# Kernel optimization log

Hardware: AMD Instinct MI355X
Metric: run time of the kernel (lower is better)

Reference implementation:

```python
import jax, jax.numpy as jnp
import numpy as np

B, S, D, H = 4, 2048, 1024, 16
DK = D // H


def setup_inputs() -> dict:
    key = jax.random.key(0)
    ks = jax.random.split(key, 12)
    std = 0.02
    inp = {
        "q": jax.random.normal(ks[0], (B, S, D), jnp.float32),
        "k": jax.random.normal(ks[1], (B, S, D), jnp.float32),
        "v": jax.random.normal(ks[2], (B, S, D), jnp.float32),
        # causal mask: 1 above diagonal (positions to be masked with -inf)
        "mask": jnp.triu(jnp.ones((S, S), jnp.int32), k=1)[None, None, :, :],
        "Wq": jax.random.normal(ks[3], (D, D), jnp.float32) * std,
        "bq": jnp.zeros((D,), jnp.float32),
        "Wk": jax.random.normal(ks[4], (D, D), jnp.float32) * std,
        "bk": jnp.zeros((D,), jnp.float32),
        "Wv": jax.random.normal(ks[5], (D, D), jnp.float32) * std,
        "bv": jnp.zeros((D,), jnp.float32),
        "Wo": jax.random.normal(ks[6], (D, D), jnp.float32) * std,
        "bo": jnp.zeros((D,), jnp.float32),
    }
    return inp


def _split_heads(x):
    b, s, d = x.shape
    return x.reshape(b, s, H, DK).transpose(0, 2, 1, 3)  # [B,H,S,DK]


def reference(q, k, v, mask, Wq, bq, Wk, bk, Wv, bv, Wo, bo):
    # linear projections (torch Linear: x @ W.T + b)
    qh = _split_heads(q @ Wq.T + bq)
    kh = _split_heads(k @ Wk.T + bk)
    vh = _split_heads(v @ Wv.T + bv)
    scale = 1.0 / jnp.sqrt(jnp.asarray(DK, qh.dtype))
    scores = jnp.einsum("bhqd,bhkd->bhqk", qh, kh) * scale
    scores = jnp.where(mask == 1, -jnp.inf, scores)
    attn = jax.nn.softmax(scores, axis=-1)
    # dropout is identity in eval mode (deterministic reference)
    out = jnp.einsum("bhqk,bhkd->bhqd", attn, vh)
    concat = out.transpose(0, 2, 1, 3).reshape(q.shape[0], -1, D)
    return concat @ Wo.T + bo
```

## Files before the change

kernel.cpp:

```cpp
#include <hip/hip_runtime.h>
#include <hip/hip_bf16.h>

#define BB  4
#define SS  2048
#define DD  1024
#define HH  16
#define DKK 64

typedef unsigned short u16;
typedef short v8s __attribute__((ext_vector_type(8)));
typedef short v4s __attribute__((ext_vector_type(4)));
typedef float v4f __attribute__((ext_vector_type(4)));
typedef float v16f __attribute__((ext_vector_type(16)));
typedef unsigned int v4u __attribute__((ext_vector_type(4)));

#define MFMA32(a, b, c) __builtin_amdgcn_mfma_f32_32x32x16_bf16(a, b, c, 0, 0, 0)

__device__ __forceinline__ u16 f2b(float x) {
  unsigned int u = __float_as_uint(x);
  unsigned int r = (u + 0x7fffu + ((u >> 16) & 1u)) >> 16;
  return (u16)r;
}

__device__ __forceinline__ unsigned int pkhalf(float a, float b) {
  return __builtin_amdgcn_perm(__float_as_uint(a), __float_as_uint(b), 0x03020706u);
}

__device__ __forceinline__ void gload16(const u16* g, u16* l) {
  __builtin_amdgcn_global_load_lds(
      (const __attribute__((address_space(1))) void*)g,
      (__attribute__((address_space(3))) void*)l, 16, 0, 0);
}

__device__ __forceinline__ void cvt8(const float* in, u16* out, size_t j) {
  const float4* p = (const float4*)(in + j * 8);
  float4 a = p[0], b = p[1];
  v8s r = {(short)f2b(a.x), (short)f2b(a.y), (short)f2b(a.z), (short)f2b(a.w),
           (short)f2b(b.x), (short)f2b(b.y), (short)f2b(b.z), (short)f2b(b.w)};
  *(v8s*)(out + j * 8) = r;
}

__global__ void cvt3(const float* __restrict__ q, const float* __restrict__ k,
                     const float* __restrict__ v, u16* __restrict__ x0,
                     u16* __restrict__ x1, u16* __restrict__ x2) {
  int i = blockIdx.x * blockDim.x + threadIdx.x;
  int which = i >> 20;
  size_t j = (size_t)(i & 0xFFFFF);
  const float* s = which == 0 ? q : (which == 1 ? k : v);
  u16* d = which == 0 ? x0 : (which == 1 ? x1 : x2);
  cvt8(s, d, j);
}

__global__ void cvtW(const float* __restrict__ a, const float* __restrict__ b,
                     const float* __restrict__ c, const float* __restrict__ d,
                     u16* __restrict__ oa, u16* __restrict__ ob,
                     u16* __restrict__ oc, u16* __restrict__ od) {
  int i = blockIdx.x * blockDim.x + threadIdx.x;
  int which = i >> 17;
  size_t j = (size_t)(i & 0x1FFFF);
  const float* s = which == 0 ? a : (which == 1 ? b : (which == 2 ? c : d));
  u16* o = which == 0 ? oa : (which == 1 ? ob : (which == 2 ? oc : od));
  cvt8(s, o, j);
}

__device__ __forceinline__ void gemm_core(
    const u16* __restrict__ A, const u16* __restrict__ Bw,
    int row0, int col0, u16* As, u16* Bs, v4f acc[4][4]) {
  const int tid = threadIdx.x;
  const int lane = tid & 63, wid = tid >> 6;
  const int wm = wid >> 1, wn = wid & 1;
  const int lr = lane & 15, lg = lane >> 4;

  v4f zero = {0.f, 0.f, 0.f, 0.f};
#pragma unroll
  for (int m = 0; m < 4; ++m)
#pragma unroll
    for (int n = 0; n < 4; ++n) acc[m][n] = zero;

  const int rowoff = wid * 8 + (lane >> 3);
  const int scol = ((lane & 7) ^ ((lane >> 3) & 7)) * 8;
  const u16* gA = A + (size_t)(row0 + rowoff) * DD + scol;
  const u16* gB = Bw + (size_t)(col0 + rowoff) * DD + scol;
  u16* lAb = As + wid * 512;
  u16* lBb = Bs + wid * 512;

#pragma unroll
  for (int i2 = 0; i2 < 4; ++i2) {
    gload16(gA + (size_t)(i2 * 32) * DD, lAb + i2 * 2048);
    gload16(gB + (size_t)(i2 * 32) * DD, lBb + i2 * 2048);
  }
  asm volatile("s_waitcnt vmcnt(0)" ::: "memory");
  __builtin_amdgcn_s_barrier();

  const int a_r0 = (wm * 64 + lr) * 64;
  const int b_r0 = (wn * 64 + lr) * 64;
  const int sl = lr & 7;

  for (int t = 0; t < 16; ++t) {
    const int buf = t & 1;
    if (t < 15) {
      const u16* nA = gA + (size_t)(t + 1) * 64;
      const u16* nB = gB + (size_t)(t + 1) * 64;
      u16* dA = lAb + (buf ^ 1) * 8192;
      u16* dB = lBb + (buf ^ 1) * 8192;
#pragma unroll
      for (int i2 = 0; i2 < 4; ++i2) {
        gload16(nA + (size_t)(i2 * 32) * DD, dA + i2 * 2048);
        gload16(nB + (size_t)(i2 * 32) * DD, dB + i2 * 2048);
      }
    }
    const u16* Ab = As + buf * 8192;
    const u16* Bb = Bs + buf * 8192;
#pragma unroll
    for (int ks = 0; ks < 2; ++ks) {
      v8s af[4], bf[4];
#pragma unroll
      for (int m = 0; m < 4; ++m)
        af[m] = *(const v8s*)(Ab + a_r0 + m * 1024 + (((ks * 4 + lg) ^ sl) * 8));
#pragma unroll
      for (int n = 0; n < 4; ++n)
        bf[n] = *(const v8s*)(Bb + b_r0 + n * 1024 + (((ks * 4 + lg) ^ sl) * 8));
#pragma unroll
      for (int m = 0; m < 4; ++m)
#pragma unroll
        for (int n = 0; n < 4; ++n)
          acc[m][n] = __builtin_amdgcn_mfma_f32_16x16x32_bf16(af[m], bf[n], acc[m][n], 0, 0, 0);
    }
    asm volatile("s_waitcnt vmcnt(0)" ::: "memory");
    __builtin_amdgcn_s_barrier();
  }
}

__global__ __launch_bounds__(256) void gemm_qkv(
    const u16* __restrict__ X0, const u16* __restrict__ X1, const u16* __restrict__ X2,
    const u16* __restrict__ Wqb, const u16* __restrict__ Wkb, const u16* __restrict__ Wvb,
    const float* __restrict__ bq, const float* __restrict__ bk, const float* __restrict__ bv,
    u16* __restrict__ Qp, u16* __restrict__ Kp, u16* __restrict__ VT, float qsc) {
  __shared__ u16 As[2][128][64];
  __shared__ u16 Bs[2][128][64];
  const int z = blockIdx.z;
  const u16* A = z == 0 ? X0 : (z == 1 ? X1 : X2);
  const u16* Bw = z == 0 ? Wqb : (z == 1 ? Wkb : Wvb);
  const float* bias = z == 0 ? bq : (z == 1 ? bk : bv);
  const float oscale = z == 0 ? qsc : 1.0f;
  const int row0 = blockIdx.x * 128, col0 = blockIdx.y * 128;

  v4f acc[4][4];
  gemm_core(A, Bw, row0, col0, &As[0][0][0], &Bs[0][0][0], acc);

  const int tid = threadIdx.x;
  const int lane = tid & 63, wid = tid >> 6;
  const int wm = wid >> 1, wn = wid & 1;
  const int lr = lane & 15, lg = lane >> 4;

  if (z < 2) {
    u16* C = z == 0 ? Qp : Kp;
#pragma unroll
    for (int n = 0; n < 4; ++n) {
      int gc = col0 + wn * 64 + n * 16 + lr;
      float bv2 = bias[gc];
#pragma unroll
      for (int m = 0; m < 4; ++m) {
        int gr0 = row0 + wm * 64 + m * 16 + lg * 4;
#pragma unroll
        for (int r = 0; r < 4; ++r)
          C[(size_t)(gr0 + r) * DD + gc] = f2b((acc[m][n][r] + bv2) * oscale);
      }
    }
  } else {
#pragma unroll
    for (int n = 0; n < 4; ++n) {
      int gc = col0 + wn * 64 + n * 16 + lr;
      float bv2 = bias[gc];
      int h = gc >> 6, dk = gc & 63;
#pragma unroll
      for (int m = 0; m < 4; ++m) {
        int gr0 = row0 + wm * 64 + m * 16 + lg * 4;
        int b = gr0 >> 11;
        int s = gr0 & 2047;
        u16* vbase = VT + (((size_t)b * HH + h) * DKK + dk) * SS + s;
#pragma unroll
        for (int r = 0; r < 4; ++r) vbase[r] = f2b(acc[m][n][r] + bv2);
      }
    }
  }
}

__global__ __launch_bounds__(256) void gemm_out(
    const u16* __restrict__ A, const u16* __restrict__ Bw,
    const float* __restrict__ bias, float* __restrict__ Cp) {
  __shared__ u16 As[2][128][64];
  __shared__ u16 Bs[2][128][64];
  const int row0 = blockIdx.x * 128, col0 = blockIdx.y * 128;

  v4f acc[4][4];
  gemm_core(A, Bw, row0, col0, &As[0][0][0], &Bs[0][0][0], acc);

  const int tid = threadIdx.x;
  const int lane = tid & 63, wid = tid >> 6;
  const int wm = wid >> 1, wn = wid & 1;
  const int lr = lane & 15, lg = lane >> 4;

#pragma unroll
  for (int n = 0; n < 4; ++n) {
    int gc = col0 + wn * 64 + n * 16 + lr;
    float bv2 = bias[gc];
#pragma unroll
    for (int m = 0; m < 4; ++m) {
      int gr0 = row0 + wm * 64 + m * 16 + lg * 4;
#pragma unroll
      for (int r = 0; r < 4; ++r)
        Cp[(size_t)(gr0 + r) * DD + gc] = acc[m][n][r] + bv2;
    }
  }
}

__device__ __forceinline__ void build_pa(const v16f& p, int hi, v8s& a0, v8s& a1) {
  unsigned int u0 = pkhalf(p[0], p[1]);
  unsigned int u1 = pkhalf(p[2], p[3]);
  unsigned int u2 = pkhalf(p[4], p[5]);
  unsigned int u3 = pkhalf(p[6], p[7]);
  unsigned int u4 = pkhalf(p[8], p[9]);
  unsigned int u5 = pkhalf(p[10], p[11]);
  unsigned int u6 = pkhalf(p[12], p[13]);
  unsigned int u7 = pkhalf(p[14], p[15]);
  unsigned int s0 = hi ? u0 : u2;
  unsigned int s1 = hi ? u1 : u3;
  unsigned int s2 = hi ? u4 : u6;
  unsigned int s3 = hi ? u5 : u7;
  unsigned int r0 = __shfl_xor(s0, 32);
  unsigned int r1 = __shfl_xor(s1, 32);
  unsigned int r2 = __shfl_xor(s2, 32);
  unsigned int r3 = __shfl_xor(s3, 32);
  v4u f0 = {hi ? r0 : u0, hi ? r1 : u1, hi ? u2 : r0, hi ? u3 : r1};
  v4u f1 = {hi ? r2 : u4, hi ? r3 : u5, hi ? u6 : r2, hi ? u7 : r3};
  a0 = __builtin_bit_cast(v8s, f0);
  a1 = __builtin_bit_cast(v8s, f1);
}

__global__ __launch_bounds__(256) void attn_fwd5(
    const u16* __restrict__ Qp, const u16* __restrict__ Kp,
    const u16* __restrict__ VT, u16* __restrict__ O) {
  __shared__ u16 Ks[128][72];
  __shared__ u16 Vs[64][136];
  const int tid = threadIdx.x;
  const int w = tid >> 6, lane = tid & 63;
  const int ql = lane & 31;
  const int hi = lane >> 5;
  const int i = blockIdx.x;
  const int dw = i >> 8, sl2 = i & 255;
  const int bh = sl2 & 63, g = sl2 >> 6;
  const int qt = (int)((0x3210674598BACDEFull >> (4 * (dw * 4 + g))) & 15);
  const int b = bh >> 4, h = bh & 15;
  const int q0 = qt * 128;
  const int qw0 = q0 + w * 32;
  const int qg = qw0 + ql;

  v8s qf[4];
  const u16* qbase = Qp + (size_t)(b * SS + qg) * DD + h * DKK + hi * 8;
#pragma unroll
  for (int ks = 0; ks < 4; ++ks) qf[ks] = *(const v8s*)(qbase + ks * 16);

  const int krow = tid >> 3, kcol = (tid & 7) * 8;
  const int vrow = tid >> 4, vcol = (tid & 15) * 8;
  const u16* gK = Kp + (size_t)(b * SS + krow) * DD + h * DKK + kcol;
  const u16* gV = VT + ((size_t)bh * DKK + vrow) * SS + vcol;

  const int nt = qt + 1;
  v8s stK[4], stV[4];
#pragma unroll
  for (int j = 0; j < 4; ++j) stK[j] = *(const v8s*)(gK + (size_t)(32 * j) * DD);
#pragma unroll
  for (int j = 0; j < 4; ++j) stV[j] = *(const v8s*)(gV + (size_t)(16 * j) * SS);

  float l = 0.f;
  v16f o0 = {0, 0, 0, 0, 0, 0, 0, 0, 0, 0, 0, 0, 0, 0, 0, 0};
  v16f o1 = o0;

  for (int t = 0; t < nt; ++t) {
    __syncthreads();
#pragma unroll
    for (int j = 0; j < 4; ++j) *(v8s*)&Ks[krow + 32 * j][kcol] = stK[j];
#pragma unroll
    for (int j = 0; j < 4; ++j) *(v8s*)&Vs[vrow + 16 * j][vcol] = stV[j];
    if (t + 1 < nt) {
      const u16* nK = gK + (size_t)(t + 1) * 128 * DD;
      const u16* nV = gV + (t + 1) * 128;
#pragma unroll
      for (int j = 0; j < 4; ++j) stK[j] = *(const v8s*)(nK + (size_t)(32 * j) * DD);
#pragma unroll
      for (int j = 0; j < 4; ++j) stV[j] = *(const v8s*)(nV + (size_t)(16 * j) * SS);
    }
    __syncthreads();
    const int kv0 = t * 128;

#pragma unroll
    for (int sub = 0; sub < 4; ++sub) {
      const int kvs = kv0 + sub * 32;
      if (kvs > qw0 + 31) break;

      v16f p = {0, 0, 0, 0, 0, 0, 0, 0, 0, 0, 0, 0, 0, 0, 0, 0};
#pragma unroll
      for (int ks = 0; ks < 4; ++ks) {
        v8s a = *(const v8s*)&Ks[sub * 32 + ql][ks * 16 + hi * 8];
        p = MFMA32(a, qf[ks], p);
      }

      if (kvs + 31 > qw0) {
#pragma unroll
        for (int r = 0; r < 16; ++r) {
          int row = (r & 3) + 8 * (r >> 2) + 4 * hi;
          if (kvs + row > qg) p[r] = -3.0e38f;
        }
      }

      float rs = 0.f;
#pragma unroll
      for (int r = 0; r < 16; ++r) {
        p[r] = exp2f(p[r]);
        rs += p[r];
      }
      l += rs;

      v8s pa0, pa1;
      build_pa(p, hi, pa0, pa1);

      __builtin_amdgcn_s_setprio(1);
      o0 = MFMA32(pa0, *(const v8s*)&Vs[ql][sub * 32 + hi * 8], o0);
      o0 = MFMA32(pa1, *(const v8s*)&Vs[ql][sub * 32 + 16 + hi * 8], o0);
      o1 = MFMA32(pa0, *(const v8s*)&Vs[32 + ql][sub * 32 + hi * 8], o1);
      o1 = MFMA32(pa1, *(const v8s*)&Vs[32 + ql][sub * 32 + 16 + hi * 8], o1);
      __builtin_amdgcn_s_setprio(0);
    }
  }

  float lt = l + __shfl_xor(l, 32);
  float linv = 1.f / lt;
#pragma unroll
  for (int r = 0; r < 16; ++r) {
    int row = (r & 3) + 8 * (r >> 2) + 4 * hi;
    float lr2 = __shfl(linv, row);
    size_t obase = (size_t)(b * SS + qw0 + row) * DD + h * DKK + ql;
    O[obase] = f2b(o0[r] * lr2);
    O[obase + 32] = f2b(o1[r] * lr2);
  }
}

extern "C" void kernel_launch(void* const* d_in, const int* in_sizes, int n_in,
                              void* d_out, int out_size, void* d_ws, size_t ws_size,
                              hipStream_t stream) {
  (void)in_sizes; (void)n_in; (void)out_size; (void)ws_size;
  const float* q  = (const float*)d_in[0];
  const float* k  = (const float*)d_in[1];
  const float* v  = (const float*)d_in[2];
  const float* Wq = (const float*)d_in[4];
  const float* bq = (const float*)d_in[5];
  const float* Wk = (const float*)d_in[6];
  const float* bk = (const float*)d_in[7];
  const float* Wv = (const float*)d_in[8];
  const float* bv = (const float*)d_in[9];
  const float* Wo = (const float*)d_in[10];
  const float* bo = (const float*)d_in[11];

  u16* base = (u16*)d_ws;
  const size_t WE = (size_t)DD * DD;
  const size_t PE = (size_t)BB * SS * DD;
  u16* Wq_b = base;
  u16* Wk_b = Wq_b + WE;
  u16* Wv_b = Wk_b + WE;
  u16* Wo_b = Wv_b + WE;
  u16* Qp = Wo_b + WE;
  u16* Kp = Qp + PE;
  u16* X2 = Kp + PE;
  u16* VT = X2 + PE;
  u16* Op = X2;

  u16* X0 = (u16*)d_out;
  u16* X1 = X0 + PE;

  const float qsc = 0.125f * 1.44269504f;

  cvtW<<<2048, 256, 0, stream>>>(Wq, Wk, Wv, Wo, Wq_b, Wk_b, Wv_b, Wo_b);
  cvt3<<<12288, 256, 0, stream>>>(q, k, v, X0, X1, X2);

  dim3 gq(64, 8, 3);
  gemm_qkv<<<gq, 256, 0, stream>>>(X0, X1, X2, Wq_b, Wk_b, Wv_b,
                                   bq, bk, bv, Qp, Kp, VT, qsc);

  attn_fwd5<<<1024, 256, 0, stream>>>(Qp, Kp, VT, Op);

  dim3 go(64, 8);
  gemm_out<<<go, 256, 0, stream>>>(Op, Wo_b, bo, (float*)d_out);
}
```

Measured before the change: 210.2 us.

## Replace QKV projection GEMM with 256x256-tile, 8-wave pipelined kernel

Swaps the 128x128-tile QKV projection GEMM for a new kernel using 256x256 tiles, 512 threads and a 128KB shared buffer. Global loads for the next K-step are issued in quarter-steps interleaved with the MFMA phases, with fine-grained waitcnt/barriers and raised wave priority around the MFMAs. This is meant to improve operand reuse and overlap loads with compute. The trade-off is a grid of only 384 blocks with one block per CU, which risks tail imbalance and lower occupancy.

Measured after the change: 210.1 us. No clear change (-0.0%).

```diff
diff --git a/kernel.cpp b/kernel.cpp
--- a/kernel.cpp
+++ b/kernel.cpp
@@ -63,6 +63,130 @@
   cvt8(s, o, j);
 }
 
+__global__ __launch_bounds__(512) void gemm_qkv256(
+    const u16* __restrict__ X0, const u16* __restrict__ X1, const u16* __restrict__ X2,
+    const u16* __restrict__ Wqb, const u16* __restrict__ Wkb, const u16* __restrict__ Wvb,
+    const float* __restrict__ bq, const float* __restrict__ bk, const float* __restrict__ bv,
+    u16* __restrict__ Qp, u16* __restrict__ Kp, u16* __restrict__ VT, float qsc) {
+  __shared__ u16 S[65536];
+  const int z = blockIdx.z;
+  const u16* A = z == 0 ? X0 : (z == 1 ? X1 : X2);
+  const u16* Bw = z == 0 ? Wqb : (z == 1 ? Wkb : Wvb);
+  const float* bias = z == 0 ? bq : (z == 1 ? bk : bv);
+  const float oscale = z == 0 ? qsc : 1.0f;
+  const int row0 = blockIdx.x * 256, col0 = blockIdx.y * 256;
+
+  const int tid = threadIdx.x;
+  const int lane = tid & 63, wid = tid >> 6;
+  const int wm = wid >> 2, wn = wid & 3;
+  const int lr = lane & 15, lg = lane >> 4;
+
+  v4f acc[8][4];
+  v4f zero = {0.f, 0.f, 0.f, 0.f};
+#pragma unroll
+  for (int i = 0; i < 8; ++i)
+#pragma unroll
+    for (int j = 0; j < 4; ++j) acc[i][j] = zero;
+
+  const int srow = tid >> 2;
+  const int schunk = (tid & 3) * 8;
+  auto stage = [&](const u16* G, int grow0, int kc, int halfbase) {
+#pragma unroll
+    for (int r2 = 0; r2 < 2; ++r2) {
+      gload16(G + (size_t)(grow0 + r2 * 128 + srow) * DD + kc + schunk,
+              S + halfbase + (r2 * 512 + wid * 64) * 8);
+    }
+  };
+
+  stage(A, row0, 0, 0);
+  stage(Bw, col0, 0, 32768);
+  stage(A, row0, 32, 8192);
+  stage(Bw, col0, 32, 32768 + 8192);
+  asm volatile("s_waitcnt vmcnt(4)" ::: "memory");
+  __builtin_amdgcn_s_barrier();
+
+  for (int t = 0; t < 16; ++t) {
+    const int buf = t & 1;
+    const int ab = buf * 16384;
+    const int bb = 32768 + buf * 16384;
+    const int nab = (buf ^ 1) * 16384;
+    const int nbb = 32768 + (buf ^ 1) * 16384;
+    const int kn = (t + 1) * 64;
+    v8s bf[4];
+#pragma unroll
+    for (int p = 0; p < 4; ++p) {
+      const int ks = p >> 1, mh = p & 1;
+      v8s af[4];
+      {
+        const u16* Ab = S + ab + ks * 8192 + (wm * 128 + mh * 64 + lr) * 32 + lg * 8;
+#pragma unroll
+        for (int i = 0; i < 4; ++i) af[i] = *(const v8s*)(Ab + i * 512);
+      }
+      if (mh == 0) {
+        const u16* Bb = S + bb + ks * 8192 + (wn * 64 + lr) * 32 + lg * 8;
+#pragma unroll
+        for (int nf = 0; nf < 4; ++nf) bf[nf] = *(const v8s*)(Bb + nf * 512);
+      }
+      if (t < 15) {
+        if (p == 0)      stage(A,  row0, kn,      nab);
+        else if (p == 1) stage(Bw, col0, kn,      nbb);
+        else if (p == 2) stage(A,  row0, kn + 32, nab + 8192);
+        else             stage(Bw, col0, kn + 32, nbb + 8192);
+      }
+      __builtin_amdgcn_s_barrier();
+      asm volatile("s_waitcnt lgkmcnt(0)" ::: "memory");
+      __builtin_amdgcn_sched_barrier(0);
+      __builtin_amdgcn_s_setprio(1);
+#pragma unroll
+      for (int i = 0; i < 4; ++i)
+#pragma unroll
+        for (int nf = 0; nf < 4; ++nf)
+          acc[mh * 4 + i][nf] = __builtin_amdgcn_mfma_f32_16x16x32_bf16(
+              af[i], bf[nf], acc[mh * 4 + i][nf], 0, 0, 0);
+      __builtin_amdgcn_s_setprio(0);
+      if (p == 1) {
+        if (t < 15) asm volatile("s_waitcnt vmcnt(4)" ::: "memory");
+        else        asm volatile("s_waitcnt vmcnt(0)" ::: "memory");
+      } else if (p == 3) {
+        if (t < 15) asm volatile("s_waitcnt vmcnt(4)" ::: "memory");
+      }
+      __builtin_amdgcn_s_barrier();
+    }
+  }
+
+  if (z < 2) {
+    u16* C = z == 0 ? Qp : Kp;
+#pragma unroll
+    for (int nf = 0; nf < 4; ++nf) {
+      int gc = col0 + wn * 64 + nf * 16 + lr;
+      float bv2 = bias[gc];
+#pragma unroll
+      for (int mf = 0; mf < 8; ++mf) {
+        int gr0 = row0 + wm * 128 + mf * 16 + lg * 4;
+#pragma unroll
+        for (int r = 0; r < 4; ++r)
+          C[(size_t)(gr0 + r) * DD + gc] = f2b((acc[mf][nf][r] + bv2) * oscale);
+      }
+    }
+  } else {
+#pragma unroll
+    for (int nf = 0; nf < 4; ++nf) {
+      int gc = col0 + wn * 64 + nf * 16 + lr;
+      float bv2 = bias[gc];
+      int h = gc >> 6, dk = gc & 63;
+#pragma unroll
+      for (int mf = 0; mf < 8; ++mf) {
+        int gr0 = row0 + wm * 128 + mf * 16 + lg * 4;
+        int b = gr0 >> 11;
+        int s = gr0 & 2047;
+        u16* vbase = VT + (((size_t)b * HH + h) * DKK + dk) * SS + s;
+#pragma unroll
+        for (int r = 0; r < 4; ++r) vbase[r] = f2b(acc[mf][nf][r] + bv2);
+      }
+    }
+  }
+}
+
 __device__ __forceinline__ void gemm_core(
     const u16* __restrict__ A, const u16* __restrict__ Bw,
     int row0, int col0, u16* As, u16* Bs, v4f acc[4][4]) {
@@ -128,61 +252,6 @@
     }
     asm volatile("s_waitcnt vmcnt(0)" ::: "memory");
     __builtin_amdgcn_s_barrier();
-  }
-}
-
-__global__ __launch_bounds__(256) void gemm_qkv(
-    const u16* __restrict__ X0, const u16* __restrict__ X1, const u16* __restrict__ X2,
-    const u16* __restrict__ Wqb, const u16* __restrict__ Wkb, const u16* __restrict__ Wvb,
-    const float* __restrict__ bq, const float* __restrict__ bk, const float* __restrict__ bv,
-    u16* __restrict__ Qp, u16* __restrict__ Kp, u16* __restrict__ VT, float qsc) {
-  __shared__ u16 As[2][128][64];
-  __shared__ u16 Bs[2][128][64];
-  const int z = blockIdx.z;
-  const u16* A = z == 0 ? X0 : (z == 1 ? X1 : X2);
-  const u16* Bw = z == 0 ? Wqb : (z == 1 ? Wkb : Wvb);
-  const float* bias = z == 0 ? bq : (z == 1 ? bk : bv);
-  const float oscale = z == 0 ? qsc : 1.0f;
-  const int row0 = blockIdx.x * 128, col0 = blockIdx.y * 128;
-
-  v4f acc[4][4];
-  gemm_core(A, Bw, row0, col0, &As[0][0][0], &Bs[0][0][0], acc);
-
-  const int tid = threadIdx.x;
-  const int lane = tid & 63, wid = tid >> 6;
-  const int wm = wid >> 1, wn = wid & 1;
-  const int lr = lane & 15, lg = lane >> 4;
-
-  if (z < 2) {
-    u16* C = z == 0 ? Qp : Kp;
-#pragma unroll
-    for (int n = 0; n < 4; ++n) {
-      int gc = col0 + wn * 64 + n * 16 + lr;
-      float bv2 = bias[gc];
-#pragma unroll
-      for (int m = 0; m < 4; ++m) {
-        int gr0 = row0 + wm * 64 + m * 16 + lg * 4;
-#pragma unroll
-        for (int r = 0; r < 4; ++r)
-          C[(size_t)(gr0 + r) * DD + gc] = f2b((acc[m][n][r] + bv2) * oscale);
-      }
-    }
-  } else {
-#pragma unroll
-    for (int n = 0; n < 4; ++n) {
-      int gc = col0 + wn * 64 + n * 16 + lr;
-      float bv2 = bias[gc];
-      int h = gc >> 6, dk = gc & 63;
-#pragma unroll
-      for (int m = 0; m < 4; ++m) {
-        int gr0 = row0 + wm * 64 + m * 16 + lg * 4;
-        int b = gr0 >> 11;
-        int s = gr0 & 2047;
-        u16* vbase = VT + (((size_t)b * HH + h) * DKK + dk) * SS + s;
-#pragma unroll
-        for (int r = 0; r < 4; ++r) vbase[r] = f2b(acc[m][n][r] + bv2);
-      }
-    }
   }
 }
 
@@ -383,9 +452,9 @@
   cvtW<<<2048, 256, 0, stream>>>(Wq, Wk, Wv, Wo, Wq_b, Wk_b, Wv_b, Wo_b);
   cvt3<<<12288, 256, 0, stream>>>(q, k, v, X0, X1, X2);
 
-  dim3 gq(64, 8, 3);
-  gemm_qkv<<<gq, 256, 0, stream>>>(X0, X1, X2, Wq_b, Wk_b, Wv_b,
-                                   bq, bk, bv, Qp, Kp, VT, qsc);
+  dim3 gq(32, 4, 3);
+  gemm_qkv256<<<gq, 512, 0, stream>>>(X0, X1, X2, Wq_b, Wk_b, Wv_b,
+                                      bq, bk, bv, Qp, Kp, VT, qsc);
 
   attn_fwd5<<<1024, 256, 0, stream>>>(Qp, Kp, VT, Op);
 
```

## Fuse fp32-to-bf16 activation conversion into QKV projection GEMM

Applied to the files above, without the earlier changes.

Removes the separate cvt3 kernel that converted q, k and v to bf16 in a workspace. The new gemm_qkvf kernel loads fp32 activations directly, converts them in registers and stores bf16 tiles to LDS, with a K-tile of 32 and a register-prefetch double buffer. This drops a full write and re-read of the bf16 activations and one launch. In exchange the A tile is now staged through registers instead of async global-to-LDS loads, the K step is smaller so there are more barriers per block, and each fp32 A tile is reread by all 8 column blocks.

Result: slower. 221.8 us (+5.5%).

```diff
diff --git a/kernel.cpp b/kernel.cpp
--- a/kernel.cpp
+++ b/kernel.cpp
@@ -38,17 +38,6 @@
   v8s r = {(short)f2b(a.x), (short)f2b(a.y), (short)f2b(a.z), (short)f2b(a.w),
            (short)f2b(b.x), (short)f2b(b.y), (short)f2b(b.z), (short)f2b(b.w)};
   *(v8s*)(out + j * 8) = r;
-}
-
-__global__ void cvt3(const float* __restrict__ q, const float* __restrict__ k,
-                     const float* __restrict__ v, u16* __restrict__ x0,
-                     u16* __restrict__ x1, u16* __restrict__ x2) {
-  int i = blockIdx.x * blockDim.x + threadIdx.x;
-  int which = i >> 20;
-  size_t j = (size_t)(i & 0xFFFFF);
-  const float* s = which == 0 ? q : (which == 1 ? k : v);
-  u16* d = which == 0 ? x0 : (which == 1 ? x1 : x2);
-  cvt8(s, d, j);
 }
 
 __global__ void cvtW(const float* __restrict__ a, const float* __restrict__ b,
@@ -63,6 +52,122 @@
   cvt8(s, o, j);
 }
 
+__global__ __launch_bounds__(256) void gemm_qkvf(
+    const float* __restrict__ Xq, const float* __restrict__ Xk, const float* __restrict__ Xv,
+    const u16* __restrict__ Wqb, const u16* __restrict__ Wkb, const u16* __restrict__ Wvb,
+    const float* __restrict__ bq, const float* __restrict__ bk, const float* __restrict__ bv,
+    u16* __restrict__ Qp, u16* __restrict__ Kp, u16* __restrict__ VT, float qsc) {
+  __shared__ u16 As[2][128][32];
+  __shared__ u16 Bs[2][128][32];
+  const int z = blockIdx.z;
+  const float* A = z == 0 ? Xq : (z == 1 ? Xk : Xv);
+  const u16* Bw = z == 0 ? Wqb : (z == 1 ? Wkb : Wvb);
+  const float* bias = z == 0 ? bq : (z == 1 ? bk : bv);
+  const float oscale = z == 0 ? qsc : 1.0f;
+  const int row0 = blockIdx.x * 128, col0 = blockIdx.y * 128;
+
+  const int tid = threadIdx.x;
+  const int lane = tid & 63, wid = tid >> 6;
+  const int wm = wid >> 1, wn = wid & 1;
+  const int lr = lane & 15, lg = lane >> 4;
+
+  v4f zero = {0.f, 0.f, 0.f, 0.f};
+  v4f acc[4][4];
+#pragma unroll
+  for (int m = 0; m < 4; ++m)
+#pragma unroll
+    for (int n = 0; n < 4; ++n) acc[m][n] = zero;
+
+  const int ar = tid >> 1, ah = tid & 1;
+  const float4* gA = (const float4*)(A + (size_t)(row0 + ar) * DD) + ah * 4;
+  const int e0 = wid * 128 + lane;
+  const int e1 = e0 + 64;
+  const u16* gB0 = Bw + (size_t)(col0 + (e0 >> 2)) * DD + (e0 & 3) * 8;
+  const u16* gB1 = Bw + (size_t)(col0 + (e1 >> 2)) * DD + (e1 & 3) * 8;
+  u16* lB0 = &Bs[0][0][0] + (2 * wid + 0) * 512;
+  u16* lB1 = &Bs[0][0][0] + (2 * wid + 1) * 512;
+
+  {
+    float4 pa0 = gA[0], pa1 = gA[1], pa2 = gA[2], pa3 = gA[3];
+    gload16(gB0, lB0);
+    gload16(gB1, lB1);
+    v8s w0 = {(short)f2b(pa0.x), (short)f2b(pa0.y), (short)f2b(pa0.z), (short)f2b(pa0.w),
+              (short)f2b(pa1.x), (short)f2b(pa1.y), (short)f2b(pa1.z), (short)f2b(pa1.w)};
+    v8s w1 = {(short)f2b(pa2.x), (short)f2b(pa2.y), (short)f2b(pa2.z), (short)f2b(pa2.w),
+              (short)f2b(pa3.x), (short)f2b(pa3.y), (short)f2b(pa3.z), (short)f2b(pa3.w)};
+    *(v8s*)&As[0][ar][ah * 16] = w0;
+    *(v8s*)&As[0][ar][ah * 16 + 8] = w1;
+  }
+  asm volatile("s_waitcnt vmcnt(0) lgkmcnt(0)" ::: "memory");
+  __builtin_amdgcn_s_barrier();
+
+  for (int t = 0; t < 32; ++t) {
+    const int buf = t & 1;
+    float4 na0{}, na1{}, na2{}, na3{};
+    if (t < 31) {
+      const float4* g = gA + (t + 1) * 8;
+      na0 = g[0]; na1 = g[1]; na2 = g[2]; na3 = g[3];
+      gload16(gB0 + (t + 1) * 32, lB0 + (buf ^ 1) * 4096);
+      gload16(gB1 + (t + 1) * 32, lB1 + (buf ^ 1) * 4096);
+    }
+
+    v8s af[4], bf[4];
+#pragma unroll
+    for (int m = 0; m < 4; ++m) af[m] = *(const v8s*)&As[buf][wm * 64 + m * 16 + lr][lg * 8];
+#pragma unroll
+    for (int n = 0; n < 4; ++n) bf[n] = *(const v8s*)&Bs[buf][wn * 64 + n * 16 + lr][lg * 8];
+#pragma unroll
+    for (int m = 0; m < 4; ++m)
+#pragma unroll
+      for (int n = 0; n < 4; ++n)
+        acc[m][n] = __builtin_amdgcn_mfma_f32_16x16x32_bf16(af[m], bf[n], acc[m][n], 0, 0, 0);
+
+    if (t < 31) {
+      v8s w0 = {(short)f2b(na0.x), (short)f2b(na0.y), (short)f2b(na0.z), (short)f2b(na0.w),
+                (short)f2b(na1.x), (short)f2b(na1.y), (short)f2b(na1.z), (short)f2b(na1.w)};
+      v8s w1 = {(short)f2b(na2.x), (short)f2b(na2.y), (short)f2b(na2.z), (short)f2b(na2.w),
+                (short)f2b(na3.x), (short)f2b(na3.y), (short)f2b(na3.z), (short)f2b(na3.w)};
+      *(v8s*)&As[buf ^ 1][ar][ah * 16] = w0;
+      *(v8s*)&As[buf ^ 1][ar][ah * 16 + 8] = w1;
+      asm volatile("s_waitcnt vmcnt(0)" ::: "memory");
+    }
+    asm volatile("s_waitcnt lgkmcnt(0)" ::: "memory");
+    __builtin_amdgcn_s_barrier();
+  }
+
+  if (z < 2) {
+    u16* C = z == 0 ? Qp : Kp;
+#pragma unroll
+    for (int n = 0; n < 4; ++n) {
+      int gc = col0 + wn * 64 + n * 16 + lr;
+      float bv2 = bias[gc];
+#pragma unroll
+      for (int m = 0; m < 4; ++m) {
+        int gr0 = row0 + wm * 64 + m * 16 + lg * 4;
+#pragma unroll
+        for (int r = 0; r < 4; ++r)
+          C[(size_t)(gr0 + r) * DD + gc] = f2b((acc[m][n][r] + bv2) * oscale);
+      }
+    }
+  } else {
+#pragma unroll
+    for (int n = 0; n < 4; ++n) {
+      int gc = col0 + wn * 64 + n * 16 + lr;
+      float bv2 = bias[gc];
+      int h = gc >> 6, dk = gc & 63;
+#pragma unroll
+      for (int m = 0; m < 4; ++m) {
+        int gr0 = row0 + wm * 64 + m * 16 + lg * 4;
+        int b = gr0 >> 11;
+        int s = gr0 & 2047;
+        u16* vbase = VT + (((size_t)b * HH + h) * DKK + dk) * SS + s;
+#pragma unroll
+        for (int r = 0; r < 4; ++r) vbase[r] = f2b(acc[m][n][r] + bv2);
+      }
+    }
+  }
+}
+
 __device__ __forceinline__ void gemm_core(
     const u16* __restrict__ A, const u16* __restrict__ Bw,
     int row0, int col0, u16* As, u16* Bs, v4f acc[4][4]) {
@@ -128,61 +233,6 @@
     }
     asm volatile("s_waitcnt vmcnt(0)" ::: "memory");
     __builtin_amdgcn_s_barrier();
-  }
-}
-
-__global__ __launch_bounds__(256) void gemm_qkv(
-    const u16* __restrict__ X0, const u16* __restrict__ X1, const u16* __restrict__ X2,
-    const u16* __restrict__ Wqb, const u16* __restrict__ Wkb, const u16* __restrict__ Wvb,
-    const float* __restrict__ bq, const float* __restrict__ bk, const float* __restrict__ bv,
-    u16* __restrict__ Qp, u16* __restrict__ Kp, u16* __restrict__ VT, float qsc) {
-  __shared__ u16 As[2][128][64];
-  __shared__ u16 Bs[2][128][64];
-  const int z = blockIdx.z;
-  const u16* A = z == 0 ? X0 : (z == 1 ? X1 : X2);
-  const u16* Bw = z == 0 ? Wqb : (z == 1 ? Wkb : Wvb);
-  const float* bias = z == 0 ? bq : (z == 1 ? bk : bv);
-  const float oscale = z == 0 ? qsc : 1.0f;
-  const int row0 = blockIdx.x * 128, col0 = blockIdx.y * 128;
-
-  v4f acc[4][4];
-  gemm_core(A, Bw, row0, col0, &As[0][0][0], &Bs[0][0][0], acc);
-
-  const int tid = threadIdx.x;
-  const int lane = tid & 63, wid = tid >> 6;
-  const int wm = wid >> 1, wn = wid & 1;
-  const int lr = lane & 15, lg = lane >> 4;
-
-  if (z < 2) {
-    u16* C = z == 0 ? Qp : Kp;
-#pragma unroll
-    for (int n = 0; n < 4; ++n) {
-      int gc = col0 + wn * 64 + n * 16 + lr;
-      float bv2 = bias[gc];
-#pragma unroll
-      for (int m = 0; m < 4; ++m) {
-        int gr0 = row0 + wm * 64 + m * 16 + lg * 4;
-#pragma unroll
-        for (int r = 0; r < 4; ++r)
-          C[(size_t)(gr0 + r) * DD + gc] = f2b((acc[m][n][r] + bv2) * oscale);
-      }
-    }
-  } else {
-#pragma unroll
-    for (int n = 0; n < 4; ++n) {
-      int gc = col0 + wn * 64 + n * 16 + lr;
-      float bv2 = bias[gc];
-      int h = gc >> 6, dk = gc & 63;
-#pragma unroll
-      for (int m = 0; m < 4; ++m) {
-        int gr0 = row0 + wm * 64 + m * 16 + lg * 4;
-        int b = gr0 >> 11;
-        int s = gr0 & 2047;
-        u16* vbase = VT + (((size_t)b * HH + h) * DKK + dk) * SS + s;
-#pragma unroll
-        for (int r = 0; r < 4; ++r) vbase[r] = f2b(acc[m][n][r] + bv2);
-      }
-    }
   }
 }
 
@@ -371,21 +421,16 @@
   u16* Wo_b = Wv_b + WE;
   u16* Qp = Wo_b + WE;
   u16* Kp = Qp + PE;
-  u16* X2 = Kp + PE;
-  u16* VT = X2 + PE;
-  u16* Op = X2;
-
-  u16* X0 = (u16*)d_out;
-  u16* X1 = X0 + PE;
+  u16* Op = Kp + PE;
+  u16* VT = Op + PE;
 
   const float qsc = 0.125f * 1.44269504f;
 
   cvtW<<<2048, 256, 0, stream>>>(Wq, Wk, Wv, Wo, Wq_b, Wk_b, Wv_b, Wo_b);
-  cvt3<<<12288, 256, 0, stream>>>(q, k, v, X0, X1, X2);
 
   dim3 gq(64, 8, 3);
-  gemm_qkv<<<gq, 256, 0, stream>>>(X0, X1, X2, Wq_b, Wk_b, Wv_b,
-                                   bq, bk, bv, Qp, Kp, VT, qsc);
+  gemm_qkvf<<<gq, 256, 0, stream>>>(q, k, v, Wq_b, Wk_b, Wv_b,
+                                    bq, bk, bv, Qp, Kp, VT, qsc);
 
   attn_fwd5<<<1024, 256, 0, stream>>>(Qp, Kp, VT, Op);
 
```
